# Kernel optimization log

Measured on AMD Instinct MI355X. Metric: run time of the kernel, lower is better.

## Reference

```python
import jax, jax.numpy as jnp
import numpy as np

B, S, D, H = 4, 2048, 1024, 16
HD = D // H  # head dim = 64


def setup_inputs() -> dict:
    key = jax.random.key(0)
    ks = jax.random.split(key, 10)
    sd = 1.0 / np.sqrt(D)
    return {
        "x": jax.random.normal(ks[0], (B, S, D), jnp.float32),
        "Wq": jax.random.normal(ks[1], (D, D), jnp.float32) * sd,
        "Wk": jax.random.normal(ks[2], (D, D), jnp.float32) * sd,
        "Wv": jax.random.normal(ks[3], (D, D), jnp.float32) * sd,
        "in_w": jax.random.normal(ks[4], (3 * D, D), jnp.float32) * sd,
        "in_b": jax.random.normal(ks[5], (3 * D,), jnp.float32) * 0.01,
        "out_w": jax.random.normal(ks[6], (D, D), jnp.float32) * sd,
        "out_b": jax.random.normal(ks[7], (D,), jnp.float32) * 0.01,
        "proj_w": jax.random.normal(ks[8], (D, D), jnp.float32) * sd,
        "proj_b": jax.random.normal(ks[9], (D,), jnp.float32) * 0.01,
    }


def _attn_block(x, Wq, Wk, Wv, in_w, in_b, out_w, out_b, proj_w, proj_b):
    b, s, d = x.shape
    # redundant pre-projections (bias-free)
    q = jnp.einsum('bsd,ed->bse', x, Wq)
    k = jnp.einsum('bsd,ed->bse', x, Wk)
    v = jnp.einsum('bsd,ed->bse', x, Wv)
    # MultiheadAttention internal in-projection (with bias)
    wq, wk, wv = in_w[:d], in_w[d:2 * d], in_w[2 * d:]
    bq, bk, bv = in_b[:d], in_b[d:2 * d], in_b[2 * d:]
    Q = jnp.einsum('bse,fe->bsf', q, wq) + bq
    K = jnp.einsum('bse,fe->bsf', k, wk) + bk
    V = jnp.einsum('bse,fe->bsf', v, wv) + bv
    # split heads -> [b, h, s, hd]
    Q = Q.reshape(b, s, H, HD).transpose(0, 2, 1, 3)
    K = K.reshape(b, s, H, HD).transpose(0, 2, 1, 3)
    V = V.reshape(b, s, H, HD).transpose(0, 2, 1, 3)
    scale = 1.0 / np.sqrt(HD)
    scores = jnp.einsum('bhqd,bhkd->bhqk', Q * scale, K)
    # FAITHFUL quirk: float tril mask (ones / zeros) is ADDED to scores,
    # exactly as torch does with a float attn_mask (not a -inf causal mask).
    mask = jnp.tril(jnp.ones((s, s), scores.dtype))
    scores = scores + mask
    A = jax.nn.softmax(scores, axis=-1)
    ctx = jnp.einsum('bhqk,bhkd->bhqd', A, V)
    ctx = ctx.transpose(0, 2, 1, 3).reshape(b, s, d)
    attn = jnp.einsum('bse,fe->bsf', ctx, out_w) + out_b  # out_proj
    out = jnp.einsum('bse,fe->bsf', attn, proj_w) + proj_b  # self.project
    return x + out


def reference(x, Wq, Wk, Wv, in_w, in_b, out_w, out_b, proj_w, proj_b):
    return _attn_block(x, Wq, Wk, Wv, in_w, in_b, out_w, out_b, proj_w, proj_b)
```

## Files before the change

kernel.cpp:

```cpp
#include <hip/hip_runtime.h>
#include <stdint.h>

typedef unsigned short u16;
typedef __attribute__((ext_vector_type(8))) short bfx8;
typedef __attribute__((ext_vector_type(4))) float fx4;
typedef __attribute__((ext_vector_type(16))) float fx16;

static __device__ __forceinline__ u16 f2b(float f) {
  union { float f; uint32_t u; } v; v.f = f;
  uint32_t r = v.u + 0x7fffu + ((v.u >> 16) & 1u);
  return (u16)(r >> 16);
}

static __device__ __forceinline__ float b2f(u16 u) {
  union { uint32_t u; float f; } v; v.u = ((uint32_t)u) << 16;
  return v.f;
}

static __device__ __forceinline__ uint32_t cvtpk(float lo, float hi) {
  uint32_t r;
  asm("v_cvt_pk_bf16_f32 %0, %1, %2" : "=v"(r) : "v"(lo), "v"(hi));
  return r;
}

static __device__ __forceinline__ float ex2(float x) {
  float r;
  asm("v_exp_f32 %0, %1" : "=v"(r) : "v"(x));
  return r;
}

static __device__ __forceinline__ void gload16(const void* g, void* lds) {
  __builtin_amdgcn_global_load_lds((const __attribute__((address_space(1))) uint32_t*)g,
                                   (__attribute__((address_space(3))) uint32_t*)lds,
                                   16, 0, 0);
}

struct Cv3 { const float* in0; u16* out0; const float* in1; u16* out1;
             const float* in2; u16* out2; };
__global__ __launch_bounds__(256) void convert3_k(Cv3 a) {
  const int b = blockIdx.x;
  const float* in; u16* out; int i;
  if (b < 4096)      { in = a.in0; out = a.out0; i = b; }
  else if (b < 5632) { in = a.in1; out = a.out1; i = b - 4096; }
  else               { in = a.in2; out = a.out2; i = b - 5632; }
  int idx = (i * 256 + threadIdx.x) * 8;
  float4 x = *(const float4*)(in + idx);
  float4 y = *(const float4*)(in + idx + 4);
  bfx8 o;
  o[0]=(short)f2b(x.x); o[1]=(short)f2b(x.y); o[2]=(short)f2b(x.z); o[3]=(short)f2b(x.w);
  o[4]=(short)f2b(y.x); o[5]=(short)f2b(y.y); o[6]=(short)f2b(y.z); o[7]=(short)f2b(y.w);
  *(bfx8*)(out + idx) = o;
}

struct TransArgs { const float* in[4]; u16* out[4]; };
__global__ __launch_bounds__(256) void transpose4_k(TransArgs ta) {
  const float* in = ta.in[blockIdx.z];
  u16* out = ta.out[blockIdx.z];
  __shared__ u16 t[64][65];
  const int bx = blockIdx.x * 64, by = blockIdx.y * 64;
  const int tid = threadIdx.x;
#pragma unroll
  for (int i = 0; i < 16; ++i) {
    int idx = tid + i * 256; int r = idx >> 6, c = idx & 63;
    t[c][r] = f2b(in[(size_t)(by + r) * 1024 + bx + c]);
  }
  __syncthreads();
#pragma unroll
  for (int i = 0; i < 16; ++i) {
    int idx = tid + i * 256; int r = idx >> 6, c = idx & 63;
    out[(size_t)(bx + r) * 1024 + by + c] = t[r][c];
  }
}

__global__ __launch_bounds__(256) void make_b2_k(const float* __restrict__ pw,
                                                 const float* __restrict__ ob,
                                                 const float* __restrict__ pb,
                                                 float* __restrict__ b2) {
  const int f = blockIdx.x, tid = threadIdx.x;
  float s = 0.f;
  for (int e = tid; e < 1024; e += 256) s += pw[(size_t)f * 1024 + e] * ob[e];
#pragma unroll
  for (int d = 1; d < 64; d <<= 1) s += __shfl_xor(s, d);
  __shared__ float red[4];
  if ((tid & 63) == 0) red[tid >> 6] = s;
  __syncthreads();
  if (tid == 0) b2[f] = red[0] + red[1] + red[2] + red[3] + pb[f];
}

static __device__ __forceinline__ void gemm_core(const u16* __restrict__ A,
                                                 const u16* __restrict__ Bt,
                                                 int K, int bm, int bn,
                                                 u16* As, u16* Bs, fx4 (&acc)[4][4]) {
  const int tid = threadIdx.x, w = tid >> 6, l = tid & 63, lm = l & 15, lk = l >> 4;
  const int wm = w >> 1, wn = w & 1;
  const int nkt = K >> 6;
  for (int kt = 0; kt < nkt; ++kt) {
#pragma unroll
    for (int i = 0; i < 4; ++i) {
      int off = i * 4096 + w * 1024;
      int loff = off + l * 16;
      int row = loff >> 7, cb = loff & 127;
      gload16((const char*)A + ((size_t)(bm * 128 + row) * K + kt * 64) * 2 + cb,
              (char*)As + off);
      gload16((const char*)Bt + ((size_t)(bn * 128 + row) * K + kt * 64) * 2 + cb,
              (char*)Bs + off);
    }
    __syncthreads();
#pragma unroll
    for (int kk = 0; kk < 2; ++kk) {
      bfx8 a[4], b[4];
#pragma unroll
      for (int mi = 0; mi < 4; ++mi)
        a[mi] = *(const bfx8*)((const char*)As + (wm * 64 + mi * 16 + lm) * 128 + lk * 16 + kk * 64);
#pragma unroll
      for (int nj = 0; nj < 4; ++nj)
        b[nj] = *(const bfx8*)((const char*)Bs + (wn * 64 + nj * 16 + lm) * 128 + lk * 16 + kk * 64);
#pragma unroll
      for (int mi = 0; mi < 4; ++mi)
#pragma unroll
        for (int nj = 0; nj < 4; ++nj)
          acc[mi][nj] = __builtin_amdgcn_mfma_f32_16x16x32_bf16(a[mi], b[nj], acc[mi][nj], 0, 0, 0);
    }
    __syncthreads();
  }
}

struct CombArgs { const u16* A[4]; const u16* Bt[4]; u16* C[4]; };
__global__ __launch_bounds__(256) void gemm_combine_k(CombArgs ca) {
  const int z = blockIdx.z;
  __shared__ u16 As[8192], Bs[8192];
  fx4 acc[4][4];
#pragma unroll
  for (int mi = 0; mi < 4; ++mi)
#pragma unroll
    for (int nj = 0; nj < 4; ++nj) acc[mi][nj] = 0.f;
  gemm_core(ca.A[z], ca.Bt[z], 1024, blockIdx.x, blockIdx.y, As, Bs, acc);
  const int tid = threadIdx.x, w = tid >> 6, l = tid & 63, lm = l & 15, lk = l >> 4;
  const int wm = w >> 1, wn = w & 1;
  u16* C = ca.C[z];
#pragma unroll
  for (int mi = 0; mi < 4; ++mi)
#pragma unroll
    for (int nj = 0; nj < 4; ++nj)
#pragma unroll
      for (int r = 0; r < 4; ++r) {
        int m = blockIdx.x * 128 + wm * 64 + mi * 16 + lk * 4 + r;
        int n = blockIdx.y * 128 + wn * 64 + nj * 16 + lm;
        C[(size_t)m * 1024 + n] = f2b(acc[mi][nj][r]);
      }
}

__global__ __launch_bounds__(256) void gemm_qkv_k(const u16* __restrict__ xb,
                                                  const u16* __restrict__ Wc,
                                                  const float* __restrict__ bias,
                                                  u16* __restrict__ Qh, u16* __restrict__ Kh,
                                                  u16* __restrict__ Vh) {
  const int bl = blockIdx.x;
  const int xcd = bl & 7, local = bl >> 3;
  const int bm = xcd * 8 + (local & 7);
  const int bn = local >> 3;
  __shared__ u16 As[8192], Bs[8192];
  fx4 acc[4][4];
#pragma unroll
  for (int mi = 0; mi < 4; ++mi)
#pragma unroll
    for (int nj = 0; nj < 4; ++nj) acc[mi][nj] = 0.f;
  gemm_core(xb, Wc, 1024, bm, bn, As, Bs, acc);
  const int tid = threadIdx.x, w = tid >> 6, l = tid & 63, lm = l & 15, lk = l >> 4;
  const int wm = w >> 1, wn = w & 1;
  const int t = bn >> 3;
  u16* dst = (t == 0) ? Qh : ((t == 1) ? Kh : Vh);
#pragma unroll
  for (int mi = 0; mi < 4; ++mi)
#pragma unroll
    for (int nj = 0; nj < 4; ++nj)
#pragma unroll
      for (int r = 0; r < 4; ++r) {
        int m = bm * 128 + wm * 64 + mi * 16 + lk * 4 + r;
        int n = bn * 128 + wn * 64 + nj * 16 + lm;
        float v = acc[mi][nj][r] + bias[n];
        int f = n & 1023, h = f >> 6, hd = f & 63, b = m >> 11, s = m & 2047;
        size_t hb = ((size_t)(b * 16 + h)) * 131072;
        size_t idx;
        if (t == 2) {
          int sl = s & 63, st = s >> 6;
          idx = hb + (size_t)st * 4096 + (size_t)(hd * 64 + (sl ^ ((hd & 7) << 3)));
        } else if (t == 1) {
          idx = hb + (size_t)s * 64 + (hd ^ ((s & 7) << 3));
        } else {
          idx = hb + (size_t)s * 64 + hd;
        }
        dst[idx] = f2b(v);
      }
}

__global__ __launch_bounds__(256) void gemm_final_k(const u16* __restrict__ ctx,
                                                    const u16* __restrict__ W2,
                                                    const float* __restrict__ b2,
                                                    const float* __restrict__ x,
                                                    const u16* __restrict__ resid16,
                                                    float* __restrict__ out) {
  const int bl = blockIdx.x;
  const int xcd = bl & 7, local = bl >> 3;
  const int bm = xcd * 8 + (local & 7);
  const int bn = local >> 3;
  __shared__ u16 As[8192], Bs[8192];
  fx4 acc[4][4];
#pragma unroll
  for (int mi = 0; mi < 4; ++mi)
#pragma unroll
    for (int nj = 0; nj < 4; ++nj) acc[mi][nj] = 0.f;
  gemm_core(ctx, W2, 1024, bm, bn, As, Bs, acc);
  const int tid = threadIdx.x, w = tid >> 6, l = tid & 63, lm = l & 15, lk = l >> 4;
  const int wm = w >> 1, wn = w & 1;
#pragma unroll
  for (int mi = 0; mi < 4; ++mi)
#pragma unroll
    for (int nj = 0; nj < 4; ++nj)
#pragma unroll
      for (int r = 0; r < 4; ++r) {
        int m = bm * 128 + wm * 64 + mi * 16 + lk * 4 + r;
        int n = bn * 128 + wn * 64 + nj * 16 + lm;
        size_t idx = (size_t)m * 1024 + n;
        float res = resid16 ? b2f(resid16[idx]) : x[idx];
        out[idx] = acc[mi][nj][r] + b2[n] + res;
      }
}

__global__ __launch_bounds__(512, 4) void attn_k(const u16* __restrict__ Qh,
                                                 const u16* __restrict__ Kh,
                                                 const u16* __restrict__ Vh,
                                                 u16* __restrict__ ctx) {
  const int bl = blockIdx.x;
  const int wk = (bl & 7) * 64 + (bl >> 3);
  const int bh = wk >> 3, qt = wk & 7;
  const int tid = threadIdx.x, w = tid >> 6, l = tid & 63;
  const int ql = l & 31, h = l >> 5;
  __shared__ __align__(16) u16 Ks[2][4096];
  __shared__ __align__(16) u16 Vs[2][4096];

  const float SC = 0.18033688011112042f;
  const float MA = 1.4426950408889634f;
  const float THR = 11.541560327111708f;

  const size_t base = (size_t)bh * 131072;
  const int qb = qt * 256 + w * 32;
  const int q = qb + ql;
  bfx8 qf[4];
  {
    const u16* qp = Qh + base + (size_t)q * 64 + 8 * h;
    qf[0] = *(const bfx8*)(qp);
    qf[1] = *(const bfx8*)(qp + 16);
    qf[2] = *(const bfx8*)(qp + 32);
    qf[3] = *(const bfx8*)(qp + 48);
  }
  float m_run = -1024.f, l_part = 0.f;
  fx16 accO[2];
  accO[0] = 0.f; accO[1] = 0.f;

  const char* Kg = (const char*)(Kh + base);
  const char* Vg = (const char*)(Vh + base);
  const int o = tid * 16;
  const int sw8 = (ql & 7) << 4;

#define STAGE(t, s)                                            \
  {                                                            \
    gload16(Kg + (size_t)(t) * 8192 + o, (char*)Ks[s] + o);    \
    gload16(Vg + (size_t)(t) * 8192 + o, (char*)Vs[s] + o);    \
  }

  STAGE(0, 0);
  asm volatile("s_waitcnt vmcnt(0)" ::: "memory");
  __builtin_amdgcn_s_barrier();
  __builtin_amdgcn_sched_barrier(0);

  int cur = 0;
  for (int kt = 0; kt < 32; ++kt) {
    if (kt + 1 < 32) STAGE(kt + 1, cur ^ 1);
    __builtin_amdgcn_sched_barrier(0);

    const char* Kc = (const char*)Ks[cur];
    const char* Vc = (const char*)Vs[cur];

    fx16 sS[2];
    sS[0] = 0.f; sS[1] = 0.f;
    __builtin_amdgcn_s_setprio(1);
#pragma unroll
    for (int ks = 0; ks < 4; ++ks) {
      bfx8 kf0 = *(const bfx8*)(Kc + (0 * 32 + ql) * 128 + (((ks << 5) | (h << 4)) ^ sw8));
      bfx8 kf1 = *(const bfx8*)(Kc + (1 * 32 + ql) * 128 + (((ks << 5) | (h << 4)) ^ sw8));
      sS[0] = __builtin_amdgcn_mfma_f32_32x32x16_bf16(kf0, qf[ks], sS[0], 0, 0, 0);
      sS[1] = __builtin_amdgcn_mfma_f32_32x32x16_bf16(kf1, qf[ks], sS[1], 0, 0, 0);
    }
    __builtin_amdgcn_s_setprio(0);

    const int dk = kt - (qb >> 6);
    {
      float cO = -m_run, cI = cO + MA;
      if (dk < 0) {
#pragma unroll
        for (int r = 0; r < 16; ++r) {
          sS[0][r] = fmaf(sS[0][r], SC, cI);
          sS[1][r] = fmaf(sS[1][r], SC, cI);
        }
      } else if (dk > 0) {
#pragma unroll
        for (int r = 0; r < 16; ++r) {
          sS[0][r] = fmaf(sS[0][r], SC, cO);
          sS[1][r] = fmaf(sS[1][r], SC, cO);
        }
      } else {
#pragma unroll
        for (int kb = 0; kb < 2; ++kb)
#pragma unroll
          for (int r = 0; r < 16; ++r) {
            int key = kt * 64 + kb * 32 + (r & 3) + 8 * (r >> 2) + 4 * h;
            sS[kb][r] = fmaf(sS[kb][r], SC, (key <= q) ? cI : cO);
          }
      }
    }
    float mx;
    {
      float m0 = fmaxf(fmaxf(sS[0][0], sS[0][1]), fmaxf(sS[0][2], sS[0][3]));
      float m1 = fmaxf(fmaxf(sS[0][4], sS[0][5]), fmaxf(sS[0][6], sS[0][7]));
      float m2 = fmaxf(fmaxf(sS[0][8], sS[0][9]), fmaxf(sS[0][10], sS[0][11]));
      float m3 = fmaxf(fmaxf(sS[0][12], sS[0][13]), fmaxf(sS[0][14], sS[0][15]));
      float m4 = fmaxf(fmaxf(sS[1][0], sS[1][1]), fmaxf(sS[1][2], sS[1][3]));
      float m5 = fmaxf(fmaxf(sS[1][4], sS[1][5]), fmaxf(sS[1][6], sS[1][7]));
      float m6 = fmaxf(fmaxf(sS[1][8], sS[1][9]), fmaxf(sS[1][10], sS[1][11]));
      float m7 = fmaxf(fmaxf(sS[1][12], sS[1][13]), fmaxf(sS[1][14], sS[1][15]));
      mx = fmaxf(fmaxf(fmaxf(m0, m1), fmaxf(m2, m3)), fmaxf(fmaxf(m4, m5), fmaxf(m6, m7)));
    }
    float full = fmaxf(mx, __shfl_xor(mx, 32));
    if (!__all(full <= THR)) {
      float d = fmaxf(full, 0.f);
      float corr = ex2(-d);
      m_run += d;
      l_part *= corr;
#pragma unroll
      for (int r = 0; r < 16; ++r) {
        int rq = (r & 3) + 8 * (r >> 2) + 4 * h;
        float cr = __shfl(corr, (l & 32) | rq);
        accO[0][r] *= cr;
        accO[1][r] *= cr;
        sS[0][r] -= d;
        sS[1][r] -= d;
      }
    }
    fx16 tt;
#pragma unroll
    for (int r = 0; r < 16; ++r) {
      sS[0][r] = ex2(sS[0][r]);
      sS[1][r] = ex2(sS[1][r]);
      tt[r] = sS[0][r] + sS[1][r];
    }
    {
      float ls0 = tt[0] + tt[8],  ls1 = tt[1] + tt[9];
      float ls2 = tt[2] + tt[10], ls3 = tt[3] + tt[11];
      float ls4 = tt[4] + tt[12], ls5 = tt[5] + tt[13];
      float ls6 = tt[6] + tt[14], ls7 = tt[7] + tt[15];
      l_part += ((ls0 + ls4) + (ls1 + ls5)) + ((ls2 + ls6) + (ls3 + ls7));
    }
    uint32_t pw[8][2];
#pragma unroll
    for (int kb = 0; kb < 2; ++kb)
#pragma unroll
      for (int gg = 0; gg < 4; ++gg) {
        pw[kb * 4 + gg][0] = cvtpk(sS[kb][4 * gg + 0], sS[kb][4 * gg + 1]);
        pw[kb * 4 + gg][1] = cvtpk(sS[kb][4 * gg + 2], sS[kb][4 * gg + 3]);
      }

    __builtin_amdgcn_s_setprio(1);
#pragma unroll
    for (int ks = 0; ks < 4; ++ks) {
      union { uint32_t u[4]; bfx8 v; } pa;
#pragma unroll
      for (int p = 0; p < 2; ++p) {
        uint32_t contrib = h ? pw[2 * ks][p] : pw[2 * ks + 1][p];
        uint32_t rcv = __shfl_xor(contrib, 32);
        pa.u[p]     = h ? rcv : pw[2 * ks][p];
        pa.u[2 + p] = h ? pw[2 * ks + 1][p] : rcv;
      }
      bfx8 vf0 = *(const bfx8*)(Vc + (0 * 32 + ql) * 128 + (((ks << 5) | (h << 4)) ^ sw8));
      bfx8 vf1 = *(const bfx8*)(Vc + (1 * 32 + ql) * 128 + (((ks << 5) | (h << 4)) ^ sw8));
      accO[0] = __builtin_amdgcn_mfma_f32_32x32x16_bf16(pa.v, vf0, accO[0], 0, 0, 0);
      accO[1] = __builtin_amdgcn_mfma_f32_32x32x16_bf16(pa.v, vf1, accO[1], 0, 0, 0);
    }
    __builtin_amdgcn_s_setprio(0);

    asm volatile("s_waitcnt vmcnt(0)" ::: "memory");
    __builtin_amdgcn_s_barrier();
    __builtin_amdgcn_sched_barrier(0);
    cur ^= 1;
  }
#undef STAGE

  float inv = 1.0f / (l_part + __shfl_xor(l_part, 32));
  const int b = bh >> 4, hcol = bh & 15;
#pragma unroll
  for (int r = 0; r < 16; ++r) {
    int rq = (r & 3) + 8 * (r >> 2) + 4 * h;
    float invq = __shfl(inv, (l & 32) | rq);
    size_t rowb = ((size_t)b * 2048 + (qb + rq)) * 1024 + hcol * 64 + ql;
    ctx[rowb]      = f2b(accO[0][r] * invq);
    ctx[rowb + 32] = f2b(accO[1][r] * invq);
  }
}

extern "C" void kernel_launch(void* const* d_in, const int* in_sizes, int n_in,
                              void* d_out, int out_size, void* d_ws, size_t ws_size,
                              hipStream_t stream) {
  (void)in_sizes; (void)n_in; (void)out_size;
  const float* x      = (const float*)d_in[0];
  const float* Wq     = (const float*)d_in[1];
  const float* Wk     = (const float*)d_in[2];
  const float* Wv     = (const float*)d_in[3];
  const float* in_w   = (const float*)d_in[4];
  const float* in_b   = (const float*)d_in[5];
  const float* out_w  = (const float*)d_in[6];
  const float* out_b  = (const float*)d_in[7];
  const float* proj_w = (const float*)d_in[8];
  const float* proj_b = (const float*)d_in[9];
  float* out = (float*)d_out;

  char* ws = (char*)d_ws;
  const size_t MB = 1ull << 20;
  u16* xb   = (u16*)(ws);
  u16* Qh   = (u16*)(ws + 16 * MB);
  u16* Kh   = (u16*)(ws + 32 * MB);
  u16* Vh   = (u16*)(ws + 48 * MB);
  u16* inwb = Kh;
  u16* tmpT = Vh;
  u16* pwb  = (u16*)(ws + 48 * MB + 8 * MB);
  u16* Wc   = (u16*)(ws + 64 * MB);
  u16* W2   = (u16*)(ws + 70 * MB);
  float* b2 = (float*)(ws + 72 * MB);
  const bool bigws = ws_size >= 90 * MB;
  u16* ctx = bigws ? (u16*)(ws + 73 * MB) : xb;
  const u16* resid16 = bigws ? xb : nullptr;

  Cv3 cv; cv.in0 = x; cv.out0 = xb; cv.in1 = in_w; cv.out1 = inwb;
  cv.in2 = proj_w; cv.out2 = pwb;
  convert3_k<<<6144, 256, 0, stream>>>(cv);

  TransArgs ta;
  ta.in[0] = Wq; ta.in[1] = Wk; ta.in[2] = Wv; ta.in[3] = out_w;
  for (int z = 0; z < 4; ++z) ta.out[z] = tmpT + (size_t)z * 1048576;
  transpose4_k<<<dim3(16, 16, 4), 256, 0, stream>>>(ta);

  CombArgs ca;
  ca.A[0] = inwb; ca.A[1] = inwb + 1048576; ca.A[2] = inwb + 2097152; ca.A[3] = pwb;
  for (int z = 0; z < 4; ++z) ca.Bt[z] = tmpT + (size_t)z * 1048576;
  ca.C[0] = Wc; ca.C[1] = Wc + 1048576; ca.C[2] = Wc + 2097152; ca.C[3] = W2;
  gemm_combine_k<<<dim3(8, 8, 4), 256, 0, stream>>>(ca);

  make_b2_k<<<1024, 256, 0, stream>>>(proj_w, out_b, proj_b, b2);

  gemm_qkv_k<<<1536, 256, 0, stream>>>(xb, Wc, in_b, Qh, Kh, Vh);
  attn_k<<<512, 512, 0, stream>>>(Qh, Kh, Vh, ctx);
  gemm_final_k<<<512, 256, 0, stream>>>(ctx, W2, b2, x, resid16, out);
}
```

Before: 270.7 us.

## Split attention key range in two halves with separate combine kernel

Adds a split-K (flash-decoding style) attention path. Each block handles half of the 2048 keys for a 256-query tile, which doubles the grid from 512 to 1024 blocks. Each half writes unnormalized bf16 partial outputs plus its row sum and running max, and a new combine kernel merges the two halves with a log-sum-exp reweighting. This buys more parallelism and CU occupancy at the price of an extra launch, extra HBM traffic for the partial outputs, and an extra bf16 rounding of the unnormalized partials. The path is only taken when the workspace is at least 124 MB.

```diff
diff --git a/kernel.cpp b/kernel.cpp
--- a/kernel.cpp
+++ b/kernel.cpp
@@ -227,6 +227,7 @@
       }
 }
 
+
 __global__ __launch_bounds__(512, 4) void attn_k(const u16* __restrict__ Qh,
                                                  const u16* __restrict__ Kh,
                                                  const u16* __restrict__ Vh,
@@ -405,6 +406,227 @@
     ctx[rowb]      = f2b(accO[0][r] * invq);
     ctx[rowb + 32] = f2b(accO[1][r] * invq);
   }
+}
+
+__global__ __launch_bounds__(512, 4) void attn_split_k(const u16* __restrict__ Qh,
+                                                       const u16* __restrict__ Kh,
+                                                       const u16* __restrict__ Vh,
+                                                       u16* __restrict__ O0,
+                                                       u16* __restrict__ O1,
+                                                       float* __restrict__ l0a,
+                                                       float* __restrict__ l1a,
+                                                       float* __restrict__ m0a,
+                                                       float* __restrict__ m1a) {
+  const int bl = blockIdx.x;
+  const int wk = (bl & 7) * 128 + (bl >> 3);
+  const int bh = wk >> 4, qt = (wk >> 1) & 7, half = wk & 1;
+  const int tid = threadIdx.x, w = tid >> 6, l = tid & 63;
+  const int ql = l & 31, h = l >> 5;
+  __shared__ __align__(16) u16 Ks[2][4096];
+  __shared__ __align__(16) u16 Vs[2][4096];
+
+  const float SC = 0.18033688011112042f;
+  const float MA = 1.4426950408889634f;
+  const float THR = 11.541560327111708f;
+
+  const size_t base = (size_t)bh * 131072;
+  const int qb = qt * 256 + w * 32;
+  const int q = qb + ql;
+  bfx8 qf[4];
+  {
+    const u16* qp = Qh + base + (size_t)q * 64 + 8 * h;
+    qf[0] = *(const bfx8*)(qp);
+    qf[1] = *(const bfx8*)(qp + 16);
+    qf[2] = *(const bfx8*)(qp + 32);
+    qf[3] = *(const bfx8*)(qp + 48);
+  }
+  float m_run = -1024.f, l_part = 0.f;
+  fx16 accO[2];
+  accO[0] = 0.f; accO[1] = 0.f;
+
+  const char* Kg = (const char*)(Kh + base) + (size_t)half * 131072;
+  const char* Vg = (const char*)(Vh + base) + (size_t)half * 131072;
+  const int o = tid * 16;
+  const int sw8 = (ql & 7) << 4;
+
+#define STAGE(t, s)                                            \
+  {                                                            \
+    gload16(Kg + (size_t)(t) * 8192 + o, (char*)Ks[s] + o);    \
+    gload16(Vg + (size_t)(t) * 8192 + o, (char*)Vs[s] + o);    \
+  }
+
+  STAGE(0, 0);
+  asm volatile("s_waitcnt vmcnt(0)" ::: "memory");
+  __builtin_amdgcn_s_barrier();
+  __builtin_amdgcn_sched_barrier(0);
+
+  int cur = 0;
+  for (int kt = 0; kt < 16; ++kt) {
+    if (kt + 1 < 16) STAGE(kt + 1, cur ^ 1);
+    __builtin_amdgcn_sched_barrier(0);
+
+    const char* Kc = (const char*)Ks[cur];
+    const char* Vc = (const char*)Vs[cur];
+    const int kt2 = half * 16 + kt;
+
+    fx16 sS[2];
+    sS[0] = 0.f; sS[1] = 0.f;
+    __builtin_amdgcn_s_setprio(1);
+#pragma unroll
+    for (int ks = 0; ks < 4; ++ks) {
+      bfx8 kf0 = *(const bfx8*)(Kc + (0 * 32 + ql) * 128 + (((ks << 5) | (h << 4)) ^ sw8));
+      bfx8 kf1 = *(const bfx8*)(Kc + (1 * 32 + ql) * 128 + (((ks << 5) | (h << 4)) ^ sw8));
+      sS[0] = __builtin_amdgcn_mfma_f32_32x32x16_bf16(kf0, qf[ks], sS[0], 0, 0, 0);
+      sS[1] = __builtin_amdgcn_mfma_f32_32x32x16_bf16(kf1, qf[ks], sS[1], 0, 0, 0);
+    }
+    __builtin_amdgcn_s_setprio(0);
+
+    const int dk = kt2 - (qb >> 6);
+    {
+      float cO = -m_run, cI = cO + MA;
+      if (dk < 0) {
+#pragma unroll
+        for (int r = 0; r < 16; ++r) {
+          sS[0][r] = fmaf(sS[0][r], SC, cI);
+          sS[1][r] = fmaf(sS[1][r], SC, cI);
+        }
+      } else if (dk > 0) {
+#pragma unroll
+        for (int r = 0; r < 16; ++r) {
+          sS[0][r] = fmaf(sS[0][r], SC, cO);
+          sS[1][r] = fmaf(sS[1][r], SC, cO);
+        }
+      } else {
+#pragma unroll
+        for (int kb = 0; kb < 2; ++kb)
+#pragma unroll
+          for (int r = 0; r < 16; ++r) {
+            int key = kt2 * 64 + kb * 32 + (r & 3) + 8 * (r >> 2) + 4 * h;
+            sS[kb][r] = fmaf(sS[kb][r], SC, (key <= q) ? cI : cO);
+          }
+      }
+    }
+    float mx;
+    {
+      float m0 = fmaxf(fmaxf(sS[0][0], sS[0][1]), fmaxf(sS[0][2], sS[0][3]));
+      float m1 = fmaxf(fmaxf(sS[0][4], sS[0][5]), fmaxf(sS[0][6], sS[0][7]));
+      float m2 = fmaxf(fmaxf(sS[0][8], sS[0][9]), fmaxf(sS[0][10], sS[0][11]));
+      float m3 = fmaxf(fmaxf(sS[0][12], sS[0][13]), fmaxf(sS[0][14], sS[0][15]));
+      float m4 = fmaxf(fmaxf(sS[1][0], sS[1][1]), fmaxf(sS[1][2], sS[1][3]));
+      float m5 = fmaxf(fmaxf(sS[1][4], sS[1][5]), fmaxf(sS[1][6], sS[1][7]));
+      float m6 = fmaxf(fmaxf(sS[1][8], sS[1][9]), fmaxf(sS[1][10], sS[1][11]));
+      float m7 = fmaxf(fmaxf(sS[1][12], sS[1][13]), fmaxf(sS[1][14], sS[1][15]));
+      mx = fmaxf(fmaxf(fmaxf(m0, m1), fmaxf(m2, m3)), fmaxf(fmaxf(m4, m5), fmaxf(m6, m7)));
+    }
+    float full = fmaxf(mx, __shfl_xor(mx, 32));
+    if (!__all(full <= THR)) {
+      float d = fmaxf(full, 0.f);
+      float corr = ex2(-d);
+      m_run += d;
+      l_part *= corr;
+#pragma unroll
+      for (int r = 0; r < 16; ++r) {
+        int rq = (r & 3) + 8 * (r >> 2) + 4 * h;
+        float cr = __shfl(corr, (l & 32) | rq);
+        accO[0][r] *= cr;
+        accO[1][r] *= cr;
+        sS[0][r] -= d;
+        sS[1][r] -= d;
+      }
+    }
+    fx16 tt;
+#pragma unroll
+    for (int r = 0; r < 16; ++r) {
+      sS[0][r] = ex2(sS[0][r]);
+      sS[1][r] = ex2(sS[1][r]);
+      tt[r] = sS[0][r] + sS[1][r];
+    }
+    {
+      float ls0 = tt[0] + tt[8],  ls1 = tt[1] + tt[9];
+      float ls2 = tt[2] + tt[10], ls3 = tt[3] + tt[11];
+      float ls4 = tt[4] + tt[12], ls5 = tt[5] + tt[13];
+      float ls6 = tt[6] + tt[14], ls7 = tt[7] + tt[15];
+      l_part += ((ls0 + ls4) + (ls1 + ls5)) + ((ls2 + ls6) + (ls3 + ls7));
+    }
+    uint32_t pw[8][2];
+#pragma unroll
+    for (int kb = 0; kb < 2; ++kb)
+#pragma unroll
+      for (int gg = 0; gg < 4; ++gg) {
+        pw[kb * 4 + gg][0] = cvtpk(sS[kb][4 * gg + 0], sS[kb][4 * gg + 1]);
+        pw[kb * 4 + gg][1] = cvtpk(sS[kb][4 * gg + 2], sS[kb][4 * gg + 3]);
+      }
+
+    __builtin_amdgcn_s_setprio(1);
+#pragma unroll
+    for (int ks = 0; ks < 4; ++ks) {
+      union { uint32_t u[4]; bfx8 v; } pa;
+#pragma unroll
+      for (int p = 0; p < 2; ++p) {
+        uint32_t contrib = h ? pw[2 * ks][p] : pw[2 * ks + 1][p];
+        uint32_t rcv = __shfl_xor(contrib, 32);
+        pa.u[p]     = h ? rcv : pw[2 * ks][p];
+        pa.u[2 + p] = h ? pw[2 * ks + 1][p] : rcv;
+      }
+      bfx8 vf0 = *(const bfx8*)(Vc + (0 * 32 + ql) * 128 + (((ks << 5) | (h << 4)) ^ sw8));
+      bfx8 vf1 = *(const bfx8*)(Vc + (1 * 32 + ql) * 128 + (((ks << 5) | (h << 4)) ^ sw8));
+      accO[0] = __builtin_amdgcn_mfma_f32_32x32x16_bf16(pa.v, vf0, accO[0], 0, 0, 0);
+      accO[1] = __builtin_amdgcn_mfma_f32_32x32x16_bf16(pa.v, vf1, accO[1], 0, 0, 0);
+    }
+    __builtin_amdgcn_s_setprio(0);
+
+    asm volatile("s_waitcnt vmcnt(0)" ::: "memory");
+    __builtin_amdgcn_s_barrier();
+    __builtin_amdgcn_sched_barrier(0);
+    cur ^= 1;
+  }
+#undef STAGE
+
+  u16* Op = half ? O1 : O0;
+  float* lo = half ? l1a : l0a;
+  float* mo = half ? m1a : m0a;
+  float lfull = l_part + __shfl_xor(l_part, 32);
+  const int b = bh >> 4, hcol = bh & 15;
+#pragma unroll
+  for (int r = 0; r < 16; ++r) {
+    int rq = (r & 3) + 8 * (r >> 2) + 4 * h;
+    size_t rowb = ((size_t)b * 2048 + (qb + rq)) * 1024 + hcol * 64 + ql;
+    Op[rowb]      = f2b(accO[0][r]);
+    Op[rowb + 32] = f2b(accO[1][r]);
+  }
+  if (h == 0) {
+    lo[(size_t)bh * 2048 + qb + ql] = lfull;
+    mo[(size_t)bh * 2048 + qb + ql] = m_run;
+  }
+}
+
+__global__ __launch_bounds__(256) void attn_combine_k(const u16* __restrict__ O0,
+                                                      const u16* __restrict__ O1,
+                                                      const float* __restrict__ l0a,
+                                                      const float* __restrict__ l1a,
+                                                      const float* __restrict__ m0a,
+                                                      const float* __restrict__ m1a,
+                                                      u16* __restrict__ ctx) {
+  int base = (blockIdx.x * 256 + threadIdx.x) * 8;
+  int row = base >> 10;
+  int d = base & 1023;
+  int b = row >> 11, s = row & 2047;
+  int bh = b * 16 + (d >> 6);
+  int iml = bh * 2048 + s;
+  float m0 = m0a[iml], m1 = m1a[iml];
+  float l0 = l0a[iml], l1 = l1a[iml];
+  float M = fmaxf(m0, m1);
+  float w0 = ex2(m0 - M), w1 = ex2(m1 - M);
+  float invL = 1.0f / fmaf(l0, w0, l1 * w1);
+  bfx8 a = *(const bfx8*)(O0 + base);
+  bfx8 c = *(const bfx8*)(O1 + base);
+  bfx8 o2;
+#pragma unroll
+  for (int i = 0; i < 8; ++i) {
+    float v = fmaf(b2f((u16)a[i]), w0, b2f((u16)c[i]) * w1) * invL;
+    o2[i] = (short)f2b(v);
+  }
+  *(bfx8*)(ctx + base) = o2;
 }
 
 extern "C" void kernel_launch(void* const* d_in, const int* in_sizes, int n_in,
@@ -438,6 +660,13 @@
   const bool bigws = ws_size >= 90 * MB;
   u16* ctx = bigws ? (u16*)(ws + 73 * MB) : xb;
   const u16* resid16 = bigws ? xb : nullptr;
+  const bool split = ws_size >= 124 * MB;
+  u16* O0   = (u16*)(ws + 89 * MB);
+  u16* O1   = (u16*)(ws + 105 * MB);
+  float* l0 = (float*)(ws + 121 * MB);
+  float* l1 = (float*)(ws + 121 * MB + 524288);
+  float* m0 = (float*)(ws + 122 * MB);
+  float* m1 = (float*)(ws + 122 * MB + 524288);
 
   Cv3 cv; cv.in0 = x; cv.out0 = xb; cv.in1 = in_w; cv.out1 = inwb;
   cv.in2 = proj_w; cv.out2 = pwb;
@@ -457,6 +686,11 @@
   make_b2_k<<<1024, 256, 0, stream>>>(proj_w, out_b, proj_b, b2);
 
   gemm_qkv_k<<<1536, 256, 0, stream>>>(xb, Wc, in_b, Qh, Kh, Vh);
-  attn_k<<<512, 512, 0, stream>>>(Qh, Kh, Vh, ctx);
+  if (split) {
+    attn_split_k<<<1024, 512, 0, stream>>>(Qh, Kh, Vh, O0, O1, l0, l1, m0, m1);
+    attn_combine_k<<<4096, 256, 0, stream>>>(O0, O1, l0, l1, m0, m1, ctx);
+  } else {
+    attn_k<<<512, 512, 0, stream>>>(Qh, Kh, Vh, ctx);
+  }
   gemm_final_k<<<512, 256, 0, stream>>>(ctx, W2, b2, x, resid16, out);
 }
```

Measured after the change: 284.0 us. +4.9%, slower.
